# Optimization experiments

Measured on AMD Instinct MI355X. Metric: run time of the kernel, lower is better.

## Reference

```python
import jax, jax.numpy as jnp
import numpy as np

OUT = 7  # adaptive max-pool output size (7x7)


def setup_inputs() -> dict:
    key = jax.random.key(0)
    k1, k2, k3, k4, k5, k6 = jax.random.split(key, 6)
    C, H, W = 512, 50, 50          # feature map (stride-16 backbone)
    h_img, w_img = 800, 800        # original image
    N = 256                        # number of ROIs
    x = jax.random.normal(k1, (1, C, H, W), dtype=jnp.float32)
    img = jax.random.normal(k2, (1, 3, h_img, w_img), dtype=jnp.float32)
    # rois: (x0, y0, w, h) in image coordinates, guaranteed in-bounds
    x0 = jax.random.uniform(k3, (N,), minval=0.0, maxval=0.5 * w_img)
    y0 = jax.random.uniform(k4, (N,), minval=0.0, maxval=0.5 * h_img)
    rw = jax.random.uniform(k5, (N,), minval=0.1 * w_img, maxval=0.45 * w_img)
    rh = jax.random.uniform(k6, (N,), minval=0.1 * h_img, maxval=0.45 * h_img)
    rois = jnp.stack([x0, y0, rw, rh], axis=1).astype(jnp.float32)
    return {"x": x, "img": img, "rois": rois}


def _ceil_div(a, b):
    return -((-a) // b)


def reference(x, img, rois):
    # Faithful to the torch module: scale rois to feature grid, truncate to int,
    # crop x[:, ry:ry+rh+1, rx:rx+rw+1] and AdaptiveMaxPool2d to 7x7.
    # AdaptiveMaxPool2d bin i over size s: [floor(i*s/OUT), ceil((i+1)*s/OUT)).
    _, C, H, W = x.shape
    h_img, w_img = img.shape[2], img.shape[3]
    wscale = W / w_img
    hscale = H / h_img
    rx = (rois[:, 0] * wscale).astype(jnp.int32)
    ry = (rois[:, 1] * hscale).astype(jnp.int32)
    rw = (rois[:, 2] * wscale).astype(jnp.int32)
    rh = (rois[:, 3] * hscale).astype(jnp.int32)
    sh = rh + 1  # crop height per ROI
    sw = rw + 1  # crop width per ROI
    N = rois.shape[0]
    p = jnp.arange(OUT)
    # per-ROI, per-bin start/end (half-open) in feature coords: [N, OUT]
    ys = ry[:, None] + (p[None, :] * sh[:, None]) // OUT
    ye = ry[:, None] + _ceil_div((p[None, :] + 1) * sh[:, None], OUT)
    xs = rx[:, None] + (p[None, :] * sw[:, None]) // OUT
    xe = rx[:, None] + _ceil_div((p[None, :] + 1) * sw[:, None], OUT)

    feat = x[0]  # [C, H, W]
    neg = jnp.array(-jnp.inf, dtype=x.dtype)

    # ---- pass 1: max over rows within each vertical bin ----
    Kh = H // OUT + 3  # max possible bin height
    kh = jnp.arange(Kh)
    row_idx = ys[:, :, None] + kh  # [N, OUT, Kh]
    valid_y = row_idx < ye[:, :, None]
    row_idx = jnp.minimum(row_idx, H - 1)
    g = feat[:, row_idx, :]  # [C, N, OUT, Kh, W]
    g = jnp.where(valid_y[None, :, :, :, None], g, neg)
    rowmax = g.max(axis=3)                 # [C, N, OUT, W]
    rowmax = jnp.moveaxis(rowmax, 0, 1)    # [N, C, OUT, W]

    # ---- pass 2: max over columns within each horizontal bin ----
    Kw = W // OUT + 3
    kw = jnp.arange(Kw)
    col_idx = xs[:, :, None] + kw  # [N, OUT, Kw]
    valid_x = col_idx < xe[:, :, None]
    col_idx = jnp.minimum(col_idx, W - 1)
    flat = col_idx.reshape(N, 1, 1, OUT * Kw)
    g2 = jnp.take_along_axis(rowmax, flat, axis=3)  # [N, C, OUT, OUT*Kw]
    g2 = g2.reshape(N, C, OUT, OUT, Kw)
    g2 = jnp.where(valid_x[:, None, None, :, :], g2, neg)
    return g2.max(axis=4)  # [N, C, OUT, OUT]
```

## Files before the change

### kernel.cpp

```cpp
#include <hip/hip_runtime.h>

#define OUTP 7
#define CCH  512
#define HF   50
#define WF   50
#define NROI 256
#define WS_NEEDED (HF * WF * CCH * sizeof(float))
#define ROWSTR (WF * 256)
#define OBSTR 258

__global__ __launch_bounds__(256) void transpose_kernel(
    const float* __restrict__ x, float* __restrict__ xt)
{
    __shared__ float tile[64][51];
    const int y  = blockIdx.x >> 3;
    const int c0 = (blockIdx.x & 7) << 6;
    const int t  = threadIdx.x;
    const int wv = t >> 6, lane = t & 63;

    for (int r = 0; r < 16; ++r) {
        const int cl = wv * 16 + r;
        if (lane < WF)
            tile[cl][lane] = x[(c0 + cl) * (HF * WF) + y * WF + lane];
    }
    __syncthreads();

    const int g   = c0 >> 8;
    const int cin = c0 & 255;
    for (int k = 0; k < 13; ++k) {
        const int xx = (t >> 6) + 4 * k;
        if (xx < WF)
            xt[((size_t)g * (HF * WF) + y * WF + xx) * 256 + cin + (t & 63)]
                = tile[t & 63][xx];
    }
}

__global__ __launch_bounds__(512) void roipool_t_kernel(
    const float* __restrict__ xt,
    const float* __restrict__ rois,
    float* __restrict__ out)
{
    __shared__ float ob[49 * OBSTR];

    const int n  = blockIdx.x >> 1;
    const int cg = blockIdx.x & 1;
    const int t  = threadIdx.x;
    const int wv = t >> 6, lane = t & 63;

    const float4 rv = *(const float4*)(rois + n * 4);
    const int rx = (int)(rv.x * 0.0625f);
    const int ry = (int)(rv.y * 0.0625f);
    const int sw = (int)(rv.z * 0.0625f) + 1;
    const int sh = (int)(rv.w * 0.0625f) + 1;

    const float* part = xt + (size_t)cg * (HF * WF * 256) + 4 * lane;

#define M4(a) { m.x = fmaxf(m.x,(a).x); m.y = fmaxf(m.y,(a).y); \
                m.z = fmaxf(m.z,(a).z); m.w = fmaxf(m.w,(a).w); }
#define LD(k) (*(const float4*)(rp + (k) * 256))

    for (int task = wv; task < 49; task += 8) {
        const int ph = task / 7;
        const int pw = task - ph * 7;
        const int ys = ry + (ph * sh) / 7;
        const int ye = ry + ((ph + 1) * sh + 6) / 7;
        const int xs = rx + (pw * sw) / 7;
        const int xe = rx + ((pw + 1) * sw + 6) / 7;
        const int yspan = ye - ys;
        const float* rp = part + (ys * WF + xs) * 256;

        float4 m = make_float4(-INFINITY, -INFINITY, -INFINITY, -INFINITY);
        switch (xe - xs) {
        case 1:
            for (int y = 0; y < yspan; ++y) { float4 a0 = LD(0); M4(a0); rp += ROWSTR; }
            break;
        case 2:
            for (int y = 0; y < yspan; ++y) { float4 a0 = LD(0), a1 = LD(1);
                M4(a0); M4(a1); rp += ROWSTR; }
            break;
        case 3:
            for (int y = 0; y < yspan; ++y) { float4 a0 = LD(0), a1 = LD(1), a2 = LD(2);
                M4(a0); M4(a1); M4(a2); rp += ROWSTR; }
            break;
        case 4:
            for (int y = 0; y < yspan; ++y) { float4 a0 = LD(0), a1 = LD(1), a2 = LD(2), a3 = LD(3);
                M4(a0); M4(a1); M4(a2); M4(a3); rp += ROWSTR; }
            break;
        default:
            for (int y = 0; y < yspan; ++y) { float4 a0 = LD(0), a1 = LD(1), a2 = LD(2), a3 = LD(3), a4 = LD(4);
                M4(a0); M4(a1); M4(a2); M4(a3); M4(a4); rp += ROWSTR; }
            break;
        }
        *(float2*)&ob[task * OBSTR + 4 * lane]     = make_float2(m.x, m.y);
        *(float2*)&ob[task * OBSTR + 4 * lane + 2] = make_float2(m.z, m.w);
    }
#undef LD
#undef M4
    __syncthreads();

    float* op = out + (size_t)(n * CCH + cg * 256) * 49;
    int c = t / 49, task = t - c * 49;
    for (int i = t; i < 256 * 49; i += 512) {
        __builtin_nontemporal_store(ob[task * OBSTR + c], &op[i]);
        task += 22; c += 10;
        if (task >= 49) { task -= 49; c += 1; }
    }
}

__global__ __launch_bounds__(256) void roipool_direct(
    const float* __restrict__ x, const float* __restrict__ rois,
    float* __restrict__ out, int total)
{
    const int stride = gridDim.x * blockDim.x;
    for (int idx = blockIdx.x * blockDim.x + threadIdx.x; idx < total; idx += stride) {
        int n = idx / (CCH * 49), rem = idx - n * (CCH * 49);
        int c = rem / 49, pp = rem - c * 49;
        int ph = pp / 7, pw = pp - ph * 7;
        const float* r = rois + n * 4;
        int rx = (int)(r[0] * 0.0625f), ry = (int)(r[1] * 0.0625f);
        int sw = (int)(r[2] * 0.0625f) + 1, sh = (int)(r[3] * 0.0625f) + 1;
        int ys = ry + (ph * sh) / 7, ye = ry + ((ph + 1) * sh + 6) / 7;
        int xs = rx + (pw * sw) / 7, xe = rx + ((pw + 1) * sw + 6) / 7;
        const float* f = x + c * (HF * WF);
        float m = -INFINITY;
        for (int y = ys; y < ye; ++y)
            for (int xx = xs; xx < xe; ++xx)
                m = fmaxf(m, f[y * WF + xx]);
        out[idx] = m;
    }
}

extern "C" void kernel_launch(void* const* d_in, const int* in_sizes, int n_in,
                              void* d_out, int out_size, void* d_ws, size_t ws_size,
                              hipStream_t stream) {
    const float* x    = (const float*)d_in[0];
    const float* rois = (const float*)d_in[2];
    float* out = (float*)d_out;

    if (ws_size >= WS_NEEDED) {
        float* xt = (float*)d_ws;
        transpose_kernel<<<HF * 8, 256, 0, stream>>>(x, xt);
        roipool_t_kernel<<<NROI * 2, 512, 0, stream>>>(xt, rois, out);
    } else {
        const int total = NROI * CCH * 49;
        roipool_direct<<<2048, 256, 0, stream>>>(x, rois, out, total);
    }
}
```

Before: 25.80 us.

## Split ROI pooling bins across two blocks and software-pipeline row loads

```diff
diff --git a/kernel.cpp b/kernel.cpp
--- a/kernel.cpp
+++ b/kernel.cpp
@@ -1,6 +1,5 @@
 #include <hip/hip_runtime.h>
 
-#define OUTP 7
 #define CCH  512
 #define HF   50
 #define WF   50
@@ -35,17 +34,20 @@
     }
 }
 
-__global__ __launch_bounds__(512) void roipool_t_kernel(
+__global__ __launch_bounds__(512, 4) void roipool_t_kernel(
     const float* __restrict__ xt,
     const float* __restrict__ rois,
     float* __restrict__ out)
 {
-    __shared__ float ob[49 * OBSTR];
+    __shared__ float ob[25 * OBSTR];
 
-    const int n  = blockIdx.x >> 1;
+    const int n  = blockIdx.x >> 2;
     const int cg = blockIdx.x & 1;
+    const int h  = (blockIdx.x >> 1) & 1;
     const int t  = threadIdx.x;
     const int wv = t >> 6, lane = t & 63;
+    const int t0 = h * 25;
+    const int cnt = 25 - h;
 
     const float4 rv = *(const float4*)(rois + n * 4);
     const int rx = (int)(rv.x * 0.0625f);
@@ -59,7 +61,7 @@
                 m.z = fmaxf(m.z,(a).z); m.w = fmaxf(m.w,(a).w); }
 #define LD(k) (*(const float4*)(rp + (k) * 256))
 
-    for (int task = wv; task < 49; task += 8) {
+    for (int task = t0 + wv; task < t0 + cnt; task += 8) {
         const int ph = task / 7;
         const int pw = task - ph * 7;
         const int ys = ry + (ph * sh) / 7;
@@ -67,43 +69,74 @@
         const int xs = rx + (pw * sw) / 7;
         const int xe = rx + ((pw + 1) * sw + 6) / 7;
         const int yspan = ye - ys;
+        const int xspan = xe - xs;
         const float* rp = part + (ys * WF + xs) * 256;
 
         float4 m = make_float4(-INFINITY, -INFINITY, -INFINITY, -INFINITY);
-        switch (xe - xs) {
-        case 1:
-            for (int y = 0; y < yspan; ++y) { float4 a0 = LD(0); M4(a0); rp += ROWSTR; }
-            break;
-        case 2:
-            for (int y = 0; y < yspan; ++y) { float4 a0 = LD(0), a1 = LD(1);
-                M4(a0); M4(a1); rp += ROWSTR; }
-            break;
-        case 3:
-            for (int y = 0; y < yspan; ++y) { float4 a0 = LD(0), a1 = LD(1), a2 = LD(2);
-                M4(a0); M4(a1); M4(a2); rp += ROWSTR; }
-            break;
-        case 4:
-            for (int y = 0; y < yspan; ++y) { float4 a0 = LD(0), a1 = LD(1), a2 = LD(2), a3 = LD(3);
-                M4(a0); M4(a1); M4(a2); M4(a3); rp += ROWSTR; }
-            break;
-        default:
-            for (int y = 0; y < yspan; ++y) { float4 a0 = LD(0), a1 = LD(1), a2 = LD(2), a3 = LD(3), a4 = LD(4);
-                M4(a0); M4(a1); M4(a2); M4(a3); M4(a4); rp += ROWSTR; }
-            break;
+        switch (xspan) {
+        case 1: {
+            float4 a0 = LD(0);
+            for (int y = 1; y < yspan; ++y) {
+                rp += ROWSTR; float4 b0 = LD(0);
+                M4(a0); a0 = b0;
+            }
+            M4(a0);
+        } break;
+        case 2: {
+            float4 a0 = LD(0), a1 = LD(1);
+            for (int y = 1; y < yspan; ++y) {
+                rp += ROWSTR; float4 b0 = LD(0), b1 = LD(1);
+                M4(a0); M4(a1); a0 = b0; a1 = b1;
+            }
+            M4(a0); M4(a1);
+        } break;
+        case 3: {
+            float4 a0 = LD(0), a1 = LD(1), a2 = LD(2);
+            for (int y = 1; y < yspan; ++y) {
+                rp += ROWSTR; float4 b0 = LD(0), b1 = LD(1), b2 = LD(2);
+                M4(a0); M4(a1); M4(a2); a0 = b0; a1 = b1; a2 = b2;
+            }
+            M4(a0); M4(a1); M4(a2);
+        } break;
+        case 4: {
+            float4 a0 = LD(0), a1 = LD(1), a2 = LD(2), a3 = LD(3);
+            for (int y = 1; y < yspan; ++y) {
+                rp += ROWSTR; float4 b0 = LD(0), b1 = LD(1), b2 = LD(2), b3 = LD(3);
+                M4(a0); M4(a1); M4(a2); M4(a3);
+                a0 = b0; a1 = b1; a2 = b2; a3 = b3;
+            }
+            M4(a0); M4(a1); M4(a2); M4(a3);
+        } break;
+        default: {
+            float4 a0 = LD(0), a1 = LD(1), a2 = LD(2), a3 = LD(3), a4 = LD(4);
+            for (int y = 1; y < yspan; ++y) {
+                rp += ROWSTR; float4 b0 = LD(0), b1 = LD(1), b2 = LD(2), b3 = LD(3), b4 = LD(4);
+                M4(a0); M4(a1); M4(a2); M4(a3); M4(a4);
+                a0 = b0; a1 = b1; a2 = b2; a3 = b3; a4 = b4;
+            }
+            M4(a0); M4(a1); M4(a2); M4(a3); M4(a4);
+        } break;
         }
-        *(float2*)&ob[task * OBSTR + 4 * lane]     = make_float2(m.x, m.y);
-        *(float2*)&ob[task * OBSTR + 4 * lane + 2] = make_float2(m.z, m.w);
+
+        const int tl = task - t0;
+        *(float2*)&ob[tl * OBSTR + 4 * lane]     = make_float2(m.x, m.y);
+        *(float2*)&ob[tl * OBSTR + 4 * lane + 2] = make_float2(m.z, m.w);
     }
 #undef LD
 #undef M4
     __syncthreads();
 
-    float* op = out + (size_t)(n * CCH + cg * 256) * 49;
-    int c = t / 49, task = t - c * 49;
-    for (int i = t; i < 256 * 49; i += 512) {
-        __builtin_nontemporal_store(ob[task * OBSTR + c], &op[i]);
-        task += 22; c += 10;
-        if (task >= 49) { task -= 49; c += 1; }
+    float* op = out + (size_t)(n * CCH + cg * 256) * 49 + t0;
+    if (h == 0) {
+        for (int i = t; i < 256 * 25; i += 512) {
+            const int c = i / 25, tl = i - c * 25;
+            __builtin_nontemporal_store(ob[tl * OBSTR + c], &op[c * 49 + tl]);
+        }
+    } else {
+        for (int i = t; i < 256 * 24; i += 512) {
+            const int c = i / 24, tl = i - c * 24;
+            __builtin_nontemporal_store(ob[tl * OBSTR + c], &op[c * 49 + tl]);
+        }
     }
 }
 
@@ -140,7 +173,7 @@
     if (ws_size >= WS_NEEDED) {
         float* xt = (float*)d_ws;
         transpose_kernel<<<HF * 8, 256, 0, stream>>>(x, xt);
-        roipool_t_kernel<<<NROI * 2, 512, 0, stream>>>(xt, rois, out);
+        roipool_t_kernel<<<NROI * 4, 512, 0, stream>>>(xt, rois, out);
     } else {
         const int total = NROI * CCH * 49;
         roipool_direct<<<2048, 256, 0, stream>>>(x, rois, out, total);
```

Measured after the change: 33.58 us. 1.3x slower.
